# Optimization experiments

Measured on AMD Instinct MI355X. Metric: run time of the kernel, lower is better.

Reference implementation:

```python
import jax, jax.numpy as jnp
import numpy as np
import math

D_MODEL, N_HEADS, D_FF = 64, 8, 256
EPS = 1e-5


def _layernorm(x, w, b):
    mu = jnp.mean(x, axis=-1, keepdims=True)
    var = jnp.mean(jnp.square(x - mu), axis=-1, keepdims=True)
    return (x - mu) * jax.lax.rsqrt(var + EPS) * w + b


def setup_inputs() -> dict:
    key = jax.random.key(0)
    ks = jax.random.split(key, 16)
    B, S, D, F = 4, 2048, D_MODEL, D_FF
    s = 1.0 / math.sqrt(D)
    inp = {
        "x": jax.random.normal(ks[0], (B, S, D), jnp.float32),
        "mask": jax.random.randint(ks[1], (B, 1, S, S), 0, 2, jnp.int32),
        "Wq": jax.random.normal(ks[2], (D, D), jnp.float32) * s,
        "bq": jax.random.normal(ks[3], (D,), jnp.float32) * 0.02,
        "Wk": jax.random.normal(ks[4], (D, D), jnp.float32) * s,
        "bk": jax.random.normal(ks[5], (D,), jnp.float32) * 0.02,
        "Wv": jax.random.normal(ks[6], (D, D), jnp.float32) * s,
        "bv": jax.random.normal(ks[7], (D,), jnp.float32) * 0.02,
        "Wo": jax.random.normal(ks[8], (D, D), jnp.float32) * s,
        "bo": jax.random.normal(ks[9], (D,), jnp.float32) * 0.02,
        "W1": jax.random.normal(ks[10], (D, F), jnp.float32) * s,
        "b1": jax.random.normal(ks[11], (F,), jnp.float32) * 0.02,
        "W2": jax.random.normal(ks[12], (F, D), jnp.float32) * (1.0 / math.sqrt(F)),
        "b2": jax.random.normal(ks[13], (D,), jnp.float32) * 0.02,
        "ln1_w": jnp.ones((D,), jnp.float32),
        "ln1_b": jnp.zeros((D,), jnp.float32),
        "ln2_w": jnp.ones((D,), jnp.float32),
        "ln2_b": jnp.zeros((D,), jnp.float32),
    }
    return inp


def reference(x, mask, Wq, bq, Wk, bk, Wv, bv, Wo, bo, W1, b1, W2, b2,
              ln1_w, ln1_b, ln2_w, ln2_b):
    B, S, D = x.shape
    H = N_HEADS
    dk = D // H

    x1 = _layernorm(x, ln1_w, ln1_b)

    # [B,S,D] -> [B,H,S,dk]
    def heads(t):
        return t.reshape(B, S, H, dk).transpose(0, 2, 1, 3)

    Q = heads(x1 @ Wq + bq)
    K = heads(x1 @ Wk + bk)
    V = heads(x1 @ Wv + bv)

    scores = jnp.einsum("bhqd,bhkd->bhqk", Q, K) / math.sqrt(dk)
    scores = jnp.where(mask == 1, jnp.float32(-1e9), scores)
    attn = jax.nn.softmax(scores, axis=-1)
    ctx = jnp.einsum("bhqk,bhkd->bhqd", attn, V)
    # Faithful to source: view [B,H,S,dk] -> [B,S,D] WITHOUT transposing heads back.
    ctx = ctx.reshape(B, S, D)
    attn_out = ctx @ Wo + bo + x1  # residual added inside attention

    x2 = x1 + attn_out  # residual added again in the block (faithful double-add)
    x3 = _layernorm(x2, ln2_w, ln2_b)
    ff = jax.nn.gelu(x3 @ W1 + b1, approximate=False) @ W2 + b2
    return x2 + ff
```

## Files before the change

kernel.cpp:

```cpp
#include <hip/hip_runtime.h>
#include <hip/hip_bf16.h>

#define SEQ 2048

typedef short s4v __attribute__((ext_vector_type(4)));
typedef float f32x4 __attribute__((ext_vector_type(4)));

using bf16 = __hip_bfloat16;
using ull = unsigned long long;

#if __has_builtin(__builtin_amdgcn_exp2f)
#define EXP2(x) __builtin_amdgcn_exp2f(x)
#else
#define EXP2(x) exp2f(x)
#endif

__device__ __forceinline__ float wred_sum(float v){
#pragma unroll
  for (int i = 1; i < 64; i <<= 1) v += __shfl_xor(v, i, 64);
  return v;
}

__device__ __forceinline__ float wred_max(float v){
#pragma unroll
  for (int i = 1; i < 64; i <<= 1) v = fmaxf(v, __shfl_xor(v, i, 64));
  return v;
}

__device__ __forceinline__ short bfs(float f){
  bf16 h = __float2bfloat16(f);
  short s;
  __builtin_memcpy(&s, &h, 2);
  return s;
}

__device__ __forceinline__ unsigned bfs2(float a, float b){
  float2 t; t.x = a; t.y = b;
  __hip_bfloat162 h = __float22bfloat162_rn(t);
  unsigned u;
  __builtin_memcpy(&u, &h, 4);
  return u;
}

__device__ __forceinline__ int detect_f32(const void* xraw){
  const unsigned short* p = (const unsigned short*)xraw;
  const int lane = threadIdx.x & 63;
  float mx = 0.f;
#pragma unroll
  for (int i = 0; i < 2; ++i){
    unsigned u = ((unsigned)p[lane * 2 + i]) << 16;
    float f = fabsf(__uint_as_float(u));
    if (!(f < 1e30f)) f = 1e30f;
    mx = fmaxf(mx, f);
  }
  mx = wred_max(mx);
  return mx > 1e3f ? 1 : 0;
}

template<int F32>
__device__ __forceinline__ float ldf(const void* p, int i){
  if constexpr (F32) return ((const float*)p)[i];
  else return __bfloat162float(((const bf16*)p)[i]);
}

#define QSCALE 0.5101129340352065f

template<int F32>
__device__ __forceinline__ void ln_qkv_body(
    const void* x,
    const void* Wq, const void* bq,
    const void* Wk, const void* bk,
    const void* Wv, const void* bv,
    const void* ln1w, const void* ln1b,
    float* x1f, bf16* Qp, bf16* Kp, bf16* Vp, float (*xs)[64])
{
  const int w = threadIdx.x >> 6, lane = threadIdx.x & 63;
  const int row = (blockIdx.x - 2048) * 4 + w;
  float xv = ldf<F32>(x, row * 64 + lane);
  float mu = wred_sum(xv) * 0.015625f;
  float dv = xv - mu;
  float var = wred_sum(dv * dv) * 0.015625f;
  float x1 = dv * rsqrtf(var + 1e-5f) * ldf<F32>(ln1w, lane) + ldf<F32>(ln1b, lane);
  x1f[(size_t)row * 64 + lane] = x1;
  xs[w][lane] = x1;
  __syncthreads();
  float q = ldf<F32>(bq, lane);
  float k = ldf<F32>(bk, lane);
  float v = ldf<F32>(bv, lane);
#pragma unroll 16
  for (int d = 0; d < 64; ++d){
    float xd = xs[w][d];
    q += xd * ldf<F32>(Wq, d * 64 + lane);
    k += xd * ldf<F32>(Wk, d * 64 + lane);
    v += xd * ldf<F32>(Wv, d * 64 + lane);
  }
  const int bq_ = row >> 11, sq = row & 2047;
  const int hh = lane >> 3, dd = lane & 7;
  const size_t pidx = (((size_t)(bq_ * 8 + hh)) * SEQ + sq) * 8 + dd;
  Qp[pidx] = __float2bfloat16(q * QSCALE);
  Kp[pidx] = __float2bfloat16(k);
  Vp[pidx] = __float2bfloat16(v);
}

template<int F32>
__device__ __forceinline__ void wt_body(
    const void* Wo, const void* W1, const void* W2,
    bf16* WoT, bf16* W1T, bf16* W2T)
{
  const int idx = (blockIdx.x - 4096) * 256 + threadIdx.x;
  if (idx < 4096){
    const int c = idx >> 6, d = idx & 63;
    WoT[idx] = __float2bfloat16(ldf<F32>(Wo, d * 64 + c));
  } else if (idx < 20480){
    const int e = idx - 4096;
    const int f = e >> 6, d = e & 63;
    W1T[e] = __float2bfloat16(ldf<F32>(W1, d * 256 + f));
  } else {
    const int e = idx - 20480;
    const int c = e >> 8, f = e & 255;
    W2T[e] = __float2bfloat16(ldf<F32>(W2, f * 64 + c));
  }
}

__global__ __launch_bounds__(256) void k_prep(
    const int* __restrict__ mask, ull* __restrict__ pm,
    const void* x, const void* Wq, const void* bq, const void* Wk, const void* bk,
    const void* Wv, const void* bv, const void* ln1w, const void* ln1b,
    float* x1f, bf16* Qp, bf16* Kp, bf16* Vp,
    const void* Wo, const void* W1, const void* W2,
    bf16* WoT, bf16* W1T, bf16* W2T)
{
  __shared__ float xs[4][64];
  const int w = threadIdx.x >> 6, lane = threadIdx.x & 63;
  if (blockIdx.x < 2048){
    const int row = blockIdx.x * 4 + w;
    const int b = row >> 11, q = row & 2047;
    const int* rp = mask + (size_t)row * SEQ;
    ull* op = pm + ((size_t)(b * 128 + (q >> 4))) * 512 + (q & 15) * 2;
#pragma unroll
    for (int it = 0; it < 8; ++it){
      const int c0 = it * 256 + lane;
      ull m0 = __ballot(rp[c0] == 1);
      ull m1 = __ballot(rp[c0 + 64] == 1);
      ull m2 = __ballot(rp[c0 + 128] == 1);
      ull m3 = __ballot(rp[c0 + 192] == 1);
      if (lane == 0){
#pragma unroll
        for (int j = 0; j < 4; ++j){
          const int wi = it * 4 + j;
          const ull mv = (j == 0) ? m0 : (j == 1) ? m1 : (j == 2) ? m2 : m3;
          op[(wi >> 1) * 32 + (wi & 1)] = mv;
        }
      }
    }
    return;
  }
  if (blockIdx.x >= 4096){
    if (detect_f32(x)) wt_body<1>(Wo, W1, W2, WoT, W1T, W2T);
    else               wt_body<0>(Wo, W1, W2, WoT, W1T, W2T);
    return;
  }
  if (detect_f32(x))
    ln_qkv_body<1>(x, Wq, bq, Wk, bk, Wv, bv, ln1w, ln1b, x1f, Qp, Kp, Vp, xs);
  else
    ln_qkv_body<0>(x, Wq, bq, Wk, bk, Wv, bv, ln1w, ln1b, x1f, Qp, Kp, Vp, xs);
}

__global__ __launch_bounds__(256) void k_vt(const bf16* __restrict__ Vp, bf16* __restrict__ Vti)
{
  const int bh = blockIdx.x >> 3;
  const int s0 = (blockIdx.x & 7) * 256;
  const int t = threadIdx.x;
  __shared__ unsigned lds[256][9];
  uint4 vrow = *reinterpret_cast<const uint4*>(Vp + ((size_t)bh * SEQ + s0 + t) * 8);
  const unsigned short* hp = (const unsigned short*)&vrow;
#pragma unroll
  for (int i = 0; i < 8; ++i) lds[t][i] = (unsigned)hp[i];
  __syncthreads();
  if (t < 144){
    const int gg = t / 9, dd = t % 9;
    unsigned short outv[16];
#pragma unroll
    for (int j = 0; j < 16; ++j)
      outv[j] = (dd < 8) ? (unsigned short)lds[gg * 16 + j][dd] : (unsigned short)0x3F80;
    uint4 o0, o1;
    o0.x = outv[0] | ((unsigned)outv[1] << 16);  o0.y = outv[2] | ((unsigned)outv[3] << 16);
    o0.z = outv[4] | ((unsigned)outv[5] << 16);  o0.w = outv[6] | ((unsigned)outv[7] << 16);
    o1.x = outv[8] | ((unsigned)outv[9] << 16);  o1.y = outv[10] | ((unsigned)outv[11] << 16);
    o1.z = outv[12] | ((unsigned)outv[13] << 16); o1.w = outv[14] | ((unsigned)outv[15] << 16);
    bf16* dst = Vti + (((size_t)(bh * 128 + (s0 >> 4) + gg)) * 9 + dd) * 16;
    *reinterpret_cast<uint4*>(dst) = o0;
    *(reinterpret_cast<uint4*>(dst) + 1) = o1;
  }
}

#define LOADT(PB, T) do {                                                          \
    const int tt_ = (T);                                                           \
    _Pragma("unroll")                                                              \
    for (int i_ = 0; i_ < 8; ++i_){                                                \
      kf[PB][i_] = *reinterpret_cast<const s4v*>(kb8 + (size_t)(tt_ * 128 + i_ * 16) * 8); \
      vf[PB][i_] = *reinterpret_cast<const s4v*>(vb8 + (size_t)(tt_ * 8 + i_) * 144);      \
    }                                                                              \
    mwv[PB] = pb[tt_ * 16];                                                        \
  } while (0)

#define COMPT(PB) do {                                                             \
    const ull mx_ = (((ull)mwv[PB].y) << 32) | mwv[PB].x;                          \
    const ull my_ = (((ull)mwv[PB].w) << 32) | mwv[PB].z;                          \
    _Pragma("unroll")                                                              \
    for (int c_ = 0; c_ < 2; ++c_){                                                \
      const ull mm_ = c_ ? my_ : mx_;                                              \
      f32x4 st_[4];                                                                \
      _Pragma("unroll")                                                            \
      for (int i_ = 0; i_ < 4; ++i_)                                               \
        st_[i_] = __builtin_amdgcn_mfma_f32_16x16x16bf16_1k(kf[PB][c_ * 4 + i_], qf, zf, 0, 0, 0); \
      _Pragma("unroll")                                                            \
      for (int i_ = 0; i_ < 4; ++i_){                                              \
        const unsigned b4_ = (unsigned)(mm_ >> (16 * i_ + sh4)) & 0xFu;            \
        float p0_ = (b4_ & 1u) ? 0.f : EXP2(st_[i_][0]);                           \
        float p1_ = (b4_ & 2u) ? 0.f : EXP2(st_[i_][1]);                           \
        float p2_ = (b4_ & 4u) ? 0.f : EXP2(st_[i_][2]);                           \
        float p3_ = (b4_ & 8u) ? 0.f : EXP2(st_[i_][3]);                           \
        union { unsigned u[2]; s4v s; } pu_;                                       \
        pu_.u[0] = bfs2(p0_, p1_);                                                 \
        pu_.u[1] = bfs2(p2_, p3_);                                                 \
        if (i_ & 1) accB = __builtin_amdgcn_mfma_f32_16x16x16bf16_1k(vf[PB][c_ * 4 + i_], pu_.s, accB, 0, 0, 0); \
        else        accA = __builtin_amdgcn_mfma_f32_16x16x16bf16_1k(vf[PB][c_ * 4 + i_], pu_.s, accA, 0, 0, 0); \
      }                                                                            \
    }                                                                              \
  } while (0)

__global__ __launch_bounds__(256, 4) void k_attn(
    const bf16* __restrict__ Qp, const bf16* __restrict__ Kp,
    const bf16* __restrict__ Vti, const uint4* __restrict__ pmi,
    bf16* __restrict__ ctxb)
{
  const int blk = blockIdx.x;
  const int hg = blk & 3;
  const int qt = (blk >> 2) & 127;
  const int b  = blk >> 9;
  const int w  = threadIdx.x >> 6;
  const int h_local = w & 1, khalf = w >> 1;
  const int h  = hg * 2 + h_local;
  const int bh = b * 8 + h;
  const int q0 = qt * 16;
  const int lane = threadIdx.x & 63;
  const int g = lane >> 4, qi = lane & 15;
  const int sh4 = 4 * g;
  const int tbase = khalf * 8;

  __shared__ float mlds[2][16][17];

  s4v qf = {0, 0, 0, 0};
  if (g < 2) qf = *reinterpret_cast<const s4v*>(Qp + ((size_t)(bh * SEQ + q0 + qi)) * 8 + sh4);

  const bf16*  kb8 = Kp + ((size_t)bh * SEQ + qi) * 8 + sh4;
  const bf16*  vb8 = Vti + (size_t)bh * 128 * 144 + qi * 16 + sh4;
  const uint4* pb  = pmi + (size_t)(b * 128 + qt) * 256 + qi;

  f32x4 accA = {0.f, 0.f, 0.f, 0.f};
  f32x4 accB = {0.f, 0.f, 0.f, 0.f};
  const f32x4 zf = {0.f, 0.f, 0.f, 0.f};

  s4v kf[2][8], vf[2][8];
  uint4 mwv[2];

  LOADT(0, tbase);
  for (int it2 = 0; it2 < 4; ++it2){
    LOADT(1, tbase + ((2 * it2 + 1) & 7));
    COMPT(0);
    LOADT(0, tbase + ((2 * it2 + 2) & 7));
    COMPT(1);
  }

  f32x4 acc;
  acc[0] = accA[0] + accB[0]; acc[1] = accA[1] + accB[1];
  acc[2] = accA[2] + accB[2]; acc[3] = accA[3] + accB[3];

  if (khalf == 1){
#pragma unroll
    for (int r = 0; r < 4; ++r) mlds[h_local][4 * g + r][qi] = acc[r];
  }
  __syncthreads();
  if (khalf == 0){
#pragma unroll
    for (int r = 0; r < 4; ++r) acc[r] += mlds[h_local][4 * g + r][qi];
    const float s = __shfl(acc[0], 32 + qi, 64);
    if (g < 2){
      const float inv = 1.f / s;
      s4v o;
      o[0] = bfs(acc[0] * inv); o[1] = bfs(acc[1] * inv);
      o[2] = bfs(acc[2] * inv); o[3] = bfs(acc[3] * inv);
      *reinterpret_cast<s4v*>(ctxb + ((size_t)(bh * SEQ + q0 + qi)) * 8 + sh4) = o;
    }
  }
}

template<int F32>
__device__ __forceinline__ void ffn_mfma_body(
    const bf16* __restrict__ ctxb, const float* __restrict__ x1f,
    const bf16* __restrict__ WoT, const bf16* __restrict__ W1T, const bf16* __restrict__ W2T,
    const void* bo, const void* b1, const void* b2,
    const void* ln2w, const void* ln2b, void* out)
{
  const int lane = threadIdx.x & 63;
  const int row0 = blockIdx.x * 16;
  const int xr = lane & 15;
  const int ko = (lane >> 4) * 4;
  const f32x4 zf = {0.f, 0.f, 0.f, 0.f};

  s4v cb[4];
#pragma unroll
  for (int kk = 0; kk < 4; ++kk)
    cb[kk] = *reinterpret_cast<const s4v*>(ctxb + (size_t)(row0 + xr) * 64 + kk * 16 + ko);

  float x2v[4][4];
#pragma unroll
  for (int t = 0; t < 4; ++t){
    f32x4 acc = zf;
#pragma unroll
    for (int kk = 0; kk < 4; ++kk){
      s4v a = *reinterpret_cast<const s4v*>(WoT + (size_t)(t * 16 + xr) * 64 + kk * 16 + ko);
      acc = __builtin_amdgcn_mfma_f32_16x16x16bf16_1k(a, cb[kk], acc, 0, 0, 0);
    }
    float4 x1q = *reinterpret_cast<const float4*>(x1f + (size_t)(row0 + xr) * 64 + t * 16 + ko);
#pragma unroll
    for (int r = 0; r < 4; ++r)
      x2v[t][r] = 2.f * (&x1q.x)[r] + acc[r] + ldf<F32>(bo, t * 16 + ko + r);
  }

  float s = 0.f;
#pragma unroll
  for (int t = 0; t < 4; ++t)
#pragma unroll
    for (int r = 0; r < 4; ++r) s += x2v[t][r];
  s += __shfl_xor(s, 16, 64);
  s += __shfl_xor(s, 32, 64);
  const float mu = s * 0.015625f;
  float vs = 0.f;
#pragma unroll
  for (int t = 0; t < 4; ++t)
#pragma unroll
    for (int r = 0; r < 4; ++r){ float d = x2v[t][r] - mu; vs += d * d; }
  vs += __shfl_xor(vs, 16, 64);
  vs += __shfl_xor(vs, 32, 64);
  const float rs = rsqrtf(vs * 0.015625f + 1e-5f);

  s4v xb[4];
#pragma unroll
  for (int t = 0; t < 4; ++t)
#pragma unroll
    for (int r = 0; r < 4; ++r)
      xb[t][r] = bfs((x2v[t][r] - mu) * rs * ldf<F32>(ln2w, t * 16 + ko + r)
                     + ldf<F32>(ln2b, t * 16 + ko + r));

  s4v gb[16];
#pragma unroll
  for (int u = 0; u < 16; ++u){
    f32x4 acc = zf;
#pragma unroll
    for (int t = 0; t < 4; ++t){
      s4v a = *reinterpret_cast<const s4v*>(W1T + (size_t)(u * 16 + xr) * 64 + t * 16 + ko);
      acc = __builtin_amdgcn_mfma_f32_16x16x16bf16_1k(a, xb[t], acc, 0, 0, 0);
    }
#pragma unroll
    for (int r = 0; r < 4; ++r){
      float h1 = acc[r] + ldf<F32>(b1, u * 16 + ko + r);
      gb[u][r] = bfs(0.5f * h1 * (1.f + erff(h1 * 0.70710678f)));
    }
  }

#pragma unroll
  for (int t = 0; t < 4; ++t){
    f32x4 acc = zf;
#pragma unroll
    for (int u = 0; u < 16; ++u){
      s4v a = *reinterpret_cast<const s4v*>(W2T + (size_t)(t * 16 + xr) * 256 + u * 16 + ko);
      acc = __builtin_amdgcn_mfma_f32_16x16x16bf16_1k(a, gb[u], acc, 0, 0, 0);
    }
    const size_t oidx = (size_t)(row0 + xr) * 64 + t * 16 + ko;
    if constexpr (F32){
      float4 o;
#pragma unroll
      for (int r = 0; r < 4; ++r)
        (&o.x)[r] = x2v[t][r] + acc[r] + ldf<F32>(b2, t * 16 + ko + r);
      *reinterpret_cast<float4*>((float*)out + oidx) = o;
    } else {
      s4v o;
#pragma unroll
      for (int r = 0; r < 4; ++r)
        o[r] = bfs(x2v[t][r] + acc[r] + ldf<F32>(b2, t * 16 + ko + r));
      *reinterpret_cast<s4v*>((bf16*)out + oidx) = o;
    }
  }
}

__global__ __launch_bounds__(64) void k_ffn(
    const void* xprobe,
    const bf16* __restrict__ ctxb, const float* __restrict__ x1f,
    const bf16* __restrict__ WoT, const bf16* __restrict__ W1T, const bf16* __restrict__ W2T,
    const void* bo, const void* b1, const void* b2,
    const void* ln2w, const void* ln2b, void* out)
{
  if (detect_f32(xprobe))
    ffn_mfma_body<1>(ctxb, x1f, WoT, W1T, W2T, bo, b1, b2, ln2w, ln2b, out);
  else
    ffn_mfma_body<0>(ctxb, x1f, WoT, W1T, W2T, bo, b1, b2, ln2w, ln2b, out);
}

extern "C" void kernel_launch(void* const* d_in, const int* in_sizes, int n_in,
                              void* d_out, int out_size, void* d_ws, size_t ws_size,
                              hipStream_t stream)
{
  (void)in_sizes; (void)n_in; (void)out_size; (void)ws_size;
  const void* x    = d_in[0];
  const int*  mask = (const int*)d_in[1];
  const void* Wq = d_in[2];
  const void* bq = d_in[3];
  const void* Wk = d_in[4];
  const void* bk = d_in[5];
  const void* Wv = d_in[6];
  const void* bv = d_in[7];
  const void* Wo = d_in[8];
  const void* bo = d_in[9];
  const void* W1 = d_in[10];
  const void* b1 = d_in[11];
  const void* W2 = d_in[12];
  const void* b2 = d_in[13];
  const void* ln1w = d_in[14];
  const void* ln1b = d_in[15];
  const void* ln2w = d_in[16];
  const void* ln2b = d_in[17];

  char* ws = (char*)d_ws;
  float* x1f = (float*)(ws + 0);
  bf16*  Qp  = (bf16*)(ws + (2u << 20));
  bf16*  Kp  = (bf16*)(ws + (3u << 20));
  bf16*  Vp  = (bf16*)(ws + (4u << 20));
  bf16*  Vti = (bf16*)(ws + (5u << 20));
  bf16*  ctxb= (bf16*)(ws + (25u << 18));
  bf16*  WoT = (bf16*)(ws + (29u << 18));
  bf16*  W1T = (bf16*)(ws + (29u << 18) + 8192);
  bf16*  W2T = (bf16*)(ws + (29u << 18) + 40960);
  ull*   pm  = (ull*)(ws + (33u << 18));

  k_prep<<<4240, 256, 0, stream>>>(mask, pm, x, Wq, bq, Wk, bk, Wv, bv, ln1w, ln1b,
                                   x1f, Qp, Kp, Vp, Wo, W1, W2, WoT, W1T, W2T);
  k_vt<<<256, 256, 0, stream>>>(Vp, Vti);
  k_attn<<<2048, 256, 0, stream>>>(Qp, Kp, Vti, (const uint4*)pm, ctxb);
  k_ffn<<<512, 64, 0, stream>>>(x, ctxb, x1f, WoT, W1T, W2T, bo, b1, b2, ln2w, ln2b, d_out);
}
```

Baseline: 97.60 us.

## Process two query tiles per attention block to reuse K/V fragments

Each attention block now handles 32 queries (two 16-row tiles) instead of 16, so every K and V fragment loaded from memory feeds twice as many MFMA operations. The grid shrinks from 2048 to 1024 blocks, and the final cross-wave reduction and normalization are duplicated per tile. The aim is to halve K/V load traffic per unit of work. In exchange it raises register pressure (more accumulators and mask words) and reduces the number of blocks available to fill the GPU.

Measured after the change: 92.66 us. 5.1% less time.

```diff
diff --git a/kernel.cpp b/kernel.cpp
--- a/kernel.cpp
+++ b/kernel.cpp
@@ -201,33 +201,39 @@
       kf[PB][i_] = *reinterpret_cast<const s4v*>(kb8 + (size_t)(tt_ * 128 + i_ * 16) * 8); \
       vf[PB][i_] = *reinterpret_cast<const s4v*>(vb8 + (size_t)(tt_ * 8 + i_) * 144);      \
     }                                                                              \
-    mwv[PB] = pb[tt_ * 16];                                                        \
+    mwvA[PB] = pbA[tt_ * 16];                                                      \
+    mwvB[PB] = pbB[tt_ * 16];                                                      \
   } while (0)
 
+#define QTILE(PB, C, MM, QF, ACCA, ACCB) do {                                      \
+    f32x4 st_[4];                                                                  \
+    _Pragma("unroll")                                                              \
+    for (int i_ = 0; i_ < 4; ++i_)                                                 \
+      st_[i_] = __builtin_amdgcn_mfma_f32_16x16x16bf16_1k(kf[PB][(C) * 4 + i_], QF, zf, 0, 0, 0); \
+    _Pragma("unroll")                                                              \
+    for (int i_ = 0; i_ < 4; ++i_){                                                \
+      const unsigned b4_ = (unsigned)((MM) >> (16 * i_ + sh4)) & 0xFu;             \
+      float p0_ = (b4_ & 1u) ? 0.f : EXP2(st_[i_][0]);                             \
+      float p1_ = (b4_ & 2u) ? 0.f : EXP2(st_[i_][1]);                             \
+      float p2_ = (b4_ & 4u) ? 0.f : EXP2(st_[i_][2]);                             \
+      float p3_ = (b4_ & 8u) ? 0.f : EXP2(st_[i_][3]);                             \
+      union { unsigned u[2]; s4v s; } pu_;                                         \
+      pu_.u[0] = bfs2(p0_, p1_);                                                   \
+      pu_.u[1] = bfs2(p2_, p3_);                                                   \
+      if (i_ & 1) ACCB = __builtin_amdgcn_mfma_f32_16x16x16bf16_1k(vf[PB][(C) * 4 + i_], pu_.s, ACCB, 0, 0, 0); \
+      else        ACCA = __builtin_amdgcn_mfma_f32_16x16x16bf16_1k(vf[PB][(C) * 4 + i_], pu_.s, ACCA, 0, 0, 0); \
+    }                                                                              \
+  } while (0)
+
 #define COMPT(PB) do {                                                             \
-    const ull mx_ = (((ull)mwv[PB].y) << 32) | mwv[PB].x;                          \
-    const ull my_ = (((ull)mwv[PB].w) << 32) | mwv[PB].z;                          \
-    _Pragma("unroll")                                                              \
-    for (int c_ = 0; c_ < 2; ++c_){                                                \
-      const ull mm_ = c_ ? my_ : mx_;                                              \
-      f32x4 st_[4];                                                                \
-      _Pragma("unroll")                                                            \
-      for (int i_ = 0; i_ < 4; ++i_)                                               \
-        st_[i_] = __builtin_amdgcn_mfma_f32_16x16x16bf16_1k(kf[PB][c_ * 4 + i_], qf, zf, 0, 0, 0); \
-      _Pragma("unroll")                                                            \
-      for (int i_ = 0; i_ < 4; ++i_){                                              \
-        const unsigned b4_ = (unsigned)(mm_ >> (16 * i_ + sh4)) & 0xFu;            \
-        float p0_ = (b4_ & 1u) ? 0.f : EXP2(st_[i_][0]);                           \
-        float p1_ = (b4_ & 2u) ? 0.f : EXP2(st_[i_][1]);                           \
-        float p2_ = (b4_ & 4u) ? 0.f : EXP2(st_[i_][2]);                           \
-        float p3_ = (b4_ & 8u) ? 0.f : EXP2(st_[i_][3]);                           \
-        union { unsigned u[2]; s4v s; } pu_;                                       \
-        pu_.u[0] = bfs2(p0_, p1_);                                                 \
-        pu_.u[1] = bfs2(p2_, p3_);                                                 \
-        if (i_ & 1) accB = __builtin_amdgcn_mfma_f32_16x16x16bf16_1k(vf[PB][c_ * 4 + i_], pu_.s, accB, 0, 0, 0); \
-        else        accA = __builtin_amdgcn_mfma_f32_16x16x16bf16_1k(vf[PB][c_ * 4 + i_], pu_.s, accA, 0, 0, 0); \
-      }                                                                            \
-    }                                                                              \
+    const ull mxA_ = (((ull)mwvA[PB].y) << 32) | mwvA[PB].x;                       \
+    const ull myA_ = (((ull)mwvA[PB].w) << 32) | mwvA[PB].z;                       \
+    const ull mxB_ = (((ull)mwvB[PB].y) << 32) | mwvB[PB].x;                       \
+    const ull myB_ = (((ull)mwvB[PB].w) << 32) | mwvB[PB].z;                       \
+    QTILE(PB, 0, mxA_, qfA, accA0, accB0);                                         \
+    QTILE(PB, 0, mxB_, qfB, accA1, accB1);                                         \
+    QTILE(PB, 1, myA_, qfA, accA0, accB0);                                         \
+    QTILE(PB, 1, myB_, qfB, accA1, accB1);                                         \
   } while (0)
 
 __global__ __launch_bounds__(256, 4) void k_attn(
@@ -237,33 +243,37 @@
 {
   const int blk = blockIdx.x;
   const int hg = blk & 3;
-  const int qt = (blk >> 2) & 127;
-  const int b  = blk >> 9;
+  const int qt = (blk >> 2) & 63;
+  const int b  = blk >> 8;
   const int w  = threadIdx.x >> 6;
   const int h_local = w & 1, khalf = w >> 1;
   const int h  = hg * 2 + h_local;
   const int bh = b * 8 + h;
-  const int q0 = qt * 16;
+  const int q0 = qt * 32;
   const int lane = threadIdx.x & 63;
   const int g = lane >> 4, qi = lane & 15;
   const int sh4 = 4 * g;
   const int tbase = khalf * 8;
 
-  __shared__ float mlds[2][16][17];
-
-  s4v qf = {0, 0, 0, 0};
-  if (g < 2) qf = *reinterpret_cast<const s4v*>(Qp + ((size_t)(bh * SEQ + q0 + qi)) * 8 + sh4);
+  __shared__ float mlds[2][2][16][17];
+
+  s4v qfA = {0, 0, 0, 0}, qfB = {0, 0, 0, 0};
+  if (g < 2){
+    qfA = *reinterpret_cast<const s4v*>(Qp + ((size_t)(bh * SEQ + q0 + qi)) * 8 + sh4);
+    qfB = *reinterpret_cast<const s4v*>(Qp + ((size_t)(bh * SEQ + q0 + 16 + qi)) * 8 + sh4);
+  }
 
   const bf16*  kb8 = Kp + ((size_t)bh * SEQ + qi) * 8 + sh4;
   const bf16*  vb8 = Vti + (size_t)bh * 128 * 144 + qi * 16 + sh4;
-  const uint4* pb  = pmi + (size_t)(b * 128 + qt) * 256 + qi;
-
-  f32x4 accA = {0.f, 0.f, 0.f, 0.f};
-  f32x4 accB = {0.f, 0.f, 0.f, 0.f};
+  const uint4* pbA = pmi + (size_t)(b * 128 + 2 * qt) * 256 + qi;
+  const uint4* pbB = pbA + 256;
+
+  f32x4 accA0 = {0.f, 0.f, 0.f, 0.f}, accB0 = {0.f, 0.f, 0.f, 0.f};
+  f32x4 accA1 = {0.f, 0.f, 0.f, 0.f}, accB1 = {0.f, 0.f, 0.f, 0.f};
   const f32x4 zf = {0.f, 0.f, 0.f, 0.f};
 
   s4v kf[2][8], vf[2][8];
-  uint4 mwv[2];
+  uint4 mwvA[2], mwvB[2];
 
   LOADT(0, tbase);
   for (int it2 = 0; it2 < 4; ++it2){
@@ -273,25 +283,36 @@
     COMPT(1);
   }
 
-  f32x4 acc;
-  acc[0] = accA[0] + accB[0]; acc[1] = accA[1] + accB[1];
-  acc[2] = accA[2] + accB[2]; acc[3] = accA[3] + accB[3];
+  f32x4 acc0, acc1;
+#pragma unroll
+  for (int r = 0; r < 4; ++r){
+    acc0[r] = accA0[r] + accB0[r];
+    acc1[r] = accA1[r] + accB1[r];
+  }
 
   if (khalf == 1){
 #pragma unroll
-    for (int r = 0; r < 4; ++r) mlds[h_local][4 * g + r][qi] = acc[r];
+    for (int r = 0; r < 4; ++r){
+      mlds[h_local][0][4 * g + r][qi] = acc0[r];
+      mlds[h_local][1][4 * g + r][qi] = acc1[r];
+    }
   }
   __syncthreads();
   if (khalf == 0){
 #pragma unroll
-    for (int r = 0; r < 4; ++r) acc[r] += mlds[h_local][4 * g + r][qi];
-    const float s = __shfl(acc[0], 32 + qi, 64);
+    for (int r = 0; r < 4; ++r){
+      acc0[r] += mlds[h_local][0][4 * g + r][qi];
+      acc1[r] += mlds[h_local][1][4 * g + r][qi];
+    }
+    const float s0 = __shfl(acc0[0], 32 + qi, 64);
+    const float s1 = __shfl(acc1[0], 32 + qi, 64);
     if (g < 2){
-      const float inv = 1.f / s;
-      s4v o;
-      o[0] = bfs(acc[0] * inv); o[1] = bfs(acc[1] * inv);
-      o[2] = bfs(acc[2] * inv); o[3] = bfs(acc[3] * inv);
-      *reinterpret_cast<s4v*>(ctxb + ((size_t)(bh * SEQ + q0 + qi)) * 8 + sh4) = o;
+      const float i0 = 1.f / s0, i1 = 1.f / s1;
+      s4v oA, oB;
+#pragma unroll
+      for (int r = 0; r < 4; ++r){ oA[r] = bfs(acc0[r] * i0); oB[r] = bfs(acc1[r] * i1); }
+      *reinterpret_cast<s4v*>(ctxb + ((size_t)(bh * SEQ + q0 + qi)) * 8 + sh4) = oA;
+      *reinterpret_cast<s4v*>(ctxb + ((size_t)(bh * SEQ + q0 + 16 + qi)) * 8 + sh4) = oB;
     }
   }
 }
@@ -447,6 +468,6 @@
   k_prep<<<4240, 256, 0, stream>>>(mask, pm, x, Wq, bq, Wk, bk, Wv, bv, ln1w, ln1b,
                                    x1f, Qp, Kp, Vp, Wo, W1, W2, WoT, W1T, W2T);
   k_vt<<<256, 256, 0, stream>>>(Vp, Vti);
-  k_attn<<<2048, 256, 0, stream>>>(Qp, Kp, Vti, (const uint4*)pm, ctxb);
+  k_attn<<<1024, 256, 0, stream>>>(Qp, Kp, Vti, (const uint4*)pm, ctxb);
   k_ffn<<<512, 64, 0, stream>>>(x, ctxb, x1f, WoT, W1T, W2T, bo, b1, b2, ln2w, ln2b, d_out);
 }
```
